# Performance work log

Hardware: AMD Instinct MI355X
Metric: run time of the kernel (lower is better)

## Reference

```python
import jax, jax.numpy as jnp
import numpy as np

N = 20000
E = 500000
IN, HID, OUT = 128, 128, 64
NEG_SLOPE = 0.01  # torch F.leaky_relu default


def setup_inputs() -> dict:
    key = jax.random.key(0)
    ks = jax.random.split(key, 16)
    d = {}
    d['x'] = jax.random.normal(ks[0], (N, IN), dtype=jnp.float32)
    # layer1 per-etype params (torch Linear convention: W is (out,in))
    d['W1_0'] = jax.random.normal(ks[1], (HID, IN), dtype=jnp.float32) / np.sqrt(IN)
    d['b1_0'] = jnp.zeros((HID,), jnp.float32)
    d['a1_0'] = jax.random.normal(ks[2], (2 * HID,), dtype=jnp.float32) / np.sqrt(2 * HID)
    d['W1_1'] = jax.random.normal(ks[3], (HID, IN), dtype=jnp.float32) / np.sqrt(IN)
    d['b1_1'] = jnp.zeros((HID,), jnp.float32)
    d['a1_1'] = jax.random.normal(ks[4], (2 * HID,), dtype=jnp.float32) / np.sqrt(2 * HID)
    # layer2 per-etype params
    d['W2_0'] = jax.random.normal(ks[5], (OUT, HID), dtype=jnp.float32) / np.sqrt(HID)
    d['b2_0'] = jnp.zeros((OUT,), jnp.float32)
    d['a2_0'] = jax.random.normal(ks[6], (2 * OUT,), dtype=jnp.float32) / np.sqrt(2 * OUT)
    d['W2_1'] = jax.random.normal(ks[7], (OUT, HID), dtype=jnp.float32) / np.sqrt(HID)
    d['b2_1'] = jnp.zeros((OUT,), jnp.float32)
    d['a2_1'] = jax.random.normal(ks[8], (2 * OUT,), dtype=jnp.float32) / np.sqrt(2 * OUT)
    # edge lists per etype
    d['src0'] = jax.random.randint(ks[9], (E,), 0, N, dtype=jnp.int32)
    d['dst0'] = jax.random.randint(ks[10], (E,), 0, N, dtype=jnp.int32)
    d['src1'] = jax.random.randint(ks[11], (E,), 0, N, dtype=jnp.int32)
    d['dst1'] = jax.random.randint(ks[12], (E,), 0, N, dtype=jnp.int32)
    return d


def _att_layer(x, Ws, bs, avs, srcs, dsts, n_nodes):
    """One AttHeteroRGCNLayer: per-etype linear + GAT attention + segment
    softmax over destination + weighted sum, then cross-etype sum."""
    h = jnp.zeros((n_nodes, Ws[0].shape[0]), x.dtype)
    for W, b, a, src, dst in zip(Ws, bs, avs, srcs, dsts):
        Wh = x @ W.T + b                       # [N, out]
        out = Wh.shape[1]
        # attn_fc(concat[Wh_src, Wh_dst]) = Wh_src@a_l + Wh_dst@a_r
        al = Wh @ a[:out]                      # [N]
        ar = Wh @ a[out:]                      # [N]
        e = jax.nn.leaky_relu(al[src] + ar[dst], NEG_SLOPE)  # [E]
        # segment softmax over incoming edges of each destination node
        m = jax.ops.segment_max(e, dst, num_segments=n_nodes)  # [N]
        ex = jnp.exp(e - m[dst])
        denom = jax.ops.segment_sum(ex, dst, num_segments=n_nodes)  # [N]
        alpha = ex / denom[dst]                # [E]
        # attention-weighted sum of gathered src messages
        h = h + jax.ops.segment_sum(alpha[:, None] * Wh[src], dst,
                                    num_segments=n_nodes)
    return h


def reference(x, W1_0, b1_0, a1_0, W1_1, b1_1, a1_1,
              W2_0, b2_0, a2_0, W2_1, b2_1, a2_1,
              src0, dst0, src1, dst1):
    srcs = [src0, src1]
    dsts = [dst0, dst1]
    h1 = _att_layer(x, [W1_0, W1_1], [b1_0, b1_1], [a1_0, a1_1], srcs, dsts, N)
    h1 = jax.nn.leaky_relu(h1, NEG_SLOPE)
    h2 = _att_layer(h1, [W2_0, W2_1], [b2_0, b2_1], [a2_0, a2_1], srcs, dsts, N)
    return h2
```

## Files before the change

### kernel.cpp

```cpp
#include <hip/hip_runtime.h>
#include <hip/hip_bf16.h>

#define NNODES 20000
#define NEDGES 500000
#define LRELU(v) ((v) > 0.f ? (v) : (v) * 0.01f)

using bf16_t = __hip_bfloat16;
typedef __attribute__((ext_vector_type(8))) short bf16x8;
typedef __attribute__((ext_vector_type(4))) float f32x4;

__device__ inline float bf2f(short u) {
  unsigned int i = ((unsigned int)(unsigned short)u) << 16;
  float f;
  __builtin_memcpy(&f, &i, 4);
  return f;
}

__global__ __launch_bounds__(256) void k_histpos(const int* __restrict__ dst0,
                                                 const int* __restrict__ dst1,
                                                 int* __restrict__ deg,
                                                 unsigned short* __restrict__ pos0,
                                                 unsigned short* __restrict__ pos1,
                                                 int ne, int n) {
  const int* dst = blockIdx.y ? dst1 : dst0;
  unsigned short* pos = blockIdx.y ? pos1 : pos0;
  int* d = deg + blockIdx.y * n;
  int i = blockIdx.x * 256 + threadIdx.x;
  if (i < ne) pos[i] = (unsigned short)atomicAdd(&d[dst[i]], 1);
}

__global__ __launch_bounds__(1024) void k_scan(const int* __restrict__ deg,
                                               int* __restrict__ row_off,
                                               int n) {
  deg += blockIdx.x * n;
  row_off += blockIdx.x * (n + 1);
  constexpr int PT = 20;
  __shared__ int wsum[16];
  int tid = threadIdx.x, wid = tid >> 6, lane = tid & 63;
  int base_i = tid * PT;
  int v[PT];
  int s = 0;
#pragma unroll
  for (int q = 0; q < PT; ++q) {
    int i = base_i + q;
    v[q] = (i < n) ? deg[i] : 0;
    s += v[q];
  }
  int x = s;
#pragma unroll
  for (int o = 1; o < 64; o <<= 1) {
    int t = __shfl_up(x, o);
    if (lane >= o) x += t;
  }
  if (lane == 63) wsum[wid] = x;
  __syncthreads();
  if (wid == 0) {
    int ws = (lane < 16) ? wsum[lane] : 0;
#pragma unroll
    for (int o = 1; o < 16; o <<= 1) {
      int t = __shfl_up(ws, o);
      if (lane >= o) ws += t;
    }
    if (lane < 16) wsum[lane] = ws;
  }
  __syncthreads();
  int run = (wid ? wsum[wid - 1] : 0) + (x - s);
#pragma unroll
  for (int q = 0; q < PT; ++q) {
    int i = base_i + q;
    if (i < n) row_off[i] = run;
    run += v[q];
  }
  if (tid == 1023) row_off[n] = run;
}

__global__ __launch_bounds__(256) void k_scatter(
    const int* __restrict__ src0, const int* __restrict__ dst0,
    const int* __restrict__ src1, const int* __restrict__ dst1,
    const unsigned short* __restrict__ pos0,
    const unsigned short* __restrict__ pos1, const int* __restrict__ row_off,
    unsigned short* __restrict__ srt0, unsigned short* __restrict__ srt1,
    int ne, int n) {
  const int* src = blockIdx.y ? src1 : src0;
  const int* dst = blockIdx.y ? dst1 : dst0;
  const unsigned short* pos = blockIdx.y ? pos1 : pos0;
  const int* ro = row_off + blockIdx.y * (n + 1);
  unsigned short* srt = blockIdx.y ? srt1 : srt0;
  int i = blockIdx.x * 256 + threadIdx.x;
  if (i < ne) {
    int dd = dst[i];
    srt[ro[dd] + (int)pos[i]] = (unsigned short)src[i];
  }
}

__global__ __launch_bounds__(256) void k_split(const float* __restrict__ in,
                                               bf16_t* __restrict__ hi,
                                               bf16_t* __restrict__ lo,
                                               int n4) {
  int i = blockIdx.x * 256 + threadIdx.x;
  if (i >= n4) return;
  float4 v = *(const float4*)&in[i * 4];
  bf16_t h0 = __float2bfloat16(v.x), h1 = __float2bfloat16(v.y);
  bf16_t h2 = __float2bfloat16(v.z), h3 = __float2bfloat16(v.w);
  hi[i * 4 + 0] = h0;
  hi[i * 4 + 1] = h1;
  hi[i * 4 + 2] = h2;
  hi[i * 4 + 3] = h3;
  lo[i * 4 + 0] = __float2bfloat16(v.x - __bfloat162float(h0));
  lo[i * 4 + 1] = __float2bfloat16(v.y - __bfloat162float(h1));
  lo[i * 4 + 2] = __float2bfloat16(v.z - __bfloat162float(h2));
  lo[i * 4 + 3] = __float2bfloat16(v.w - __bfloat162float(h3));
}

template <int F>
__global__ __launch_bounds__(256) void k_gemm_mfma(
    const bf16_t* __restrict__ Xh, const bf16_t* __restrict__ Xl,
    const bf16_t* __restrict__ Wh0, const bf16_t* __restrict__ Wl0,
    const bf16_t* __restrict__ Wh1, const bf16_t* __restrict__ Wl1,
    const float* __restrict__ b0p, const float* __restrict__ b1p,
    const float* __restrict__ a0p, const float* __restrict__ a1p,
    bf16_t* __restrict__ Y0, bf16_t* __restrict__ Y1, float* __restrict__ al0,
    float* __restrict__ ar0, float* __restrict__ al1, float* __restrict__ ar1,
    int nrows) {
  constexpr int NT = F / 16;
  int t = blockIdx.y;
  const bf16_t* Wgh = t ? Wh1 : Wh0;
  const bf16_t* Wgl = t ? Wl1 : Wl0;
  const float* bias = t ? b1p : b0p;
  const float* av = t ? a1p : a0p;
  bf16_t* Y = t ? Y1 : Y0;
  float* al = t ? al1 : al0;
  float* ar = t ? ar1 : ar0;

  int wid = threadIdx.x >> 6, lane = threadIdx.x & 63;
  int row0 = blockIdx.x * 64 + wid * 16;
  int cl = lane & 15, g4 = lane >> 4;
  int rA = row0 + cl;
  int rAc = min(rA, nrows - 1);

  f32x4 acc[NT] = {};

#pragma unroll
  for (int ks = 0; ks < 4; ++ks) {
    int k0 = ks * 32 + g4 * 8;
    bf16x8 Ah = *(const bf16x8*)&Xh[(size_t)rAc * 128 + k0];
    bf16x8 Al = *(const bf16x8*)&Xl[(size_t)rAc * 128 + k0];
#pragma unroll
    for (int nt = 0; nt < NT; ++nt) {
      size_t off = (size_t)(nt * 16 + cl) * 128 + k0;
      bf16x8 Bh = *(const bf16x8*)&Wgh[off];
      bf16x8 Bl = *(const bf16x8*)&Wgl[off];
      acc[nt] = __builtin_amdgcn_mfma_f32_16x16x32_bf16(Ah, Bh, acc[nt], 0, 0, 0);
      acc[nt] = __builtin_amdgcn_mfma_f32_16x16x32_bf16(Ah, Bl, acc[nt], 0, 0, 0);
      acc[nt] = __builtin_amdgcn_mfma_f32_16x16x32_bf16(Al, Bh, acc[nt], 0, 0, 0);
    }
  }

  float pl[4] = {}, pr[4] = {};
#pragma unroll
  for (int nt = 0; nt < NT; ++nt) {
    int c = nt * 16 + cl;
    float bv = bias[c], aL = av[c], aR = av[F + c];
#pragma unroll
    for (int j = 0; j < 4; ++j) {
      int r = row0 + g4 * 4 + j;
      float v = acc[nt][j] + bv;
      if (r < nrows) Y[(size_t)r * F + c] = __float2bfloat16(v);
      pl[j] += v * aL;
      pr[j] += v * aR;
    }
  }
#pragma unroll
  for (int j = 0; j < 4; ++j) {
    float sl = pl[j], sr = pr[j];
#pragma unroll
    for (int o = 8; o; o >>= 1) {
      sl += __shfl_xor(sl, o);
      sr += __shfl_xor(sr, o);
    }
    int r = row0 + g4 * 4 + j;
    if (cl == 0 && r < nrows) {
      al[r] = sl;
      ar[r] = sr;
    }
  }
}

template <int F, int OMODE>
__global__ __launch_bounds__(256) void k_agg2(
    const int* __restrict__ row_off, const unsigned short* __restrict__ srt0,
    const unsigned short* __restrict__ srt1, const float* __restrict__ al0,
    const float* __restrict__ ar0, const float* __restrict__ al1,
    const float* __restrict__ ar1, const bf16_t* __restrict__ Wg0,
    const bf16_t* __restrict__ Wg1, float* __restrict__ H,
    bf16_t* __restrict__ Hh, bf16_t* __restrict__ Hl, int n) {
  constexpr int LPR = (F * 2) / 16;
  constexpr int NGR = 64 / LPR;
  constexpr int VE = F / LPR;
  int wid = threadIdx.x >> 6, lane = threadIdx.x & 63;
  int d = blockIdx.x * 4 + wid;
  if (d >= n) return;
  int g = lane / LPR, cl = lane % LPR;
  float acc[VE] = {};

#pragma unroll
  for (int t = 0; t < 2; ++t) {
    const int* ro = row_off + t * (n + 1);
    const unsigned short* srt = t ? srt1 : srt0;
    const float* al = t ? al1 : al0;
    const float* ar = t ? ar1 : ar0;
    const bf16_t* Wg = t ? Wg1 : Wg0;
    int beg = ro[d], end = ro[d + 1];
    if (beg == end) continue;
    float ard = ar[d];

    float denT = 0.f;
    float accT[VE] = {};
    int j = beg + g;
    for (; j + NGR < end; j += 2 * NGR) {
      int s0 = srt[j], s1 = srt[j + NGR];
      float e0 = fminf(LRELU(al[s0] + ard), 70.f);
      float e1 = fminf(LRELU(al[s1] + ard), 70.f);
      float w0 = __expf(e0), w1 = __expf(e1);
      denT += w0 + w1;
      bf16x8 r0 = *(const bf16x8*)&Wg[(size_t)s0 * F + cl * 8];
      bf16x8 r1 = *(const bf16x8*)&Wg[(size_t)s1 * F + cl * 8];
#pragma unroll
      for (int v = 0; v < VE; ++v)
        accT[v] += w0 * bf2f(r0[v]) + w1 * bf2f(r1[v]);
    }
    if (j < end) {
      int s0 = srt[j];
      float e0 = fminf(LRELU(al[s0] + ard), 70.f);
      float w0 = __expf(e0);
      denT += w0;
      bf16x8 r0 = *(const bf16x8*)&Wg[(size_t)s0 * F + cl * 8];
#pragma unroll
      for (int v = 0; v < VE; ++v) accT[v] += w0 * bf2f(r0[v]);
    }

#pragma unroll
    for (int o = 32; o >= LPR; o >>= 1) {
      denT += __shfl_xor(denT, o);
#pragma unroll
      for (int v = 0; v < VE; ++v) accT[v] += __shfl_xor(accT[v], o);
    }
    float rden = 1.f / denT;
#pragma unroll
    for (int v = 0; v < VE; ++v) acc[v] += accT[v] * rden;
  }

  if (g == 0) {
    if (OMODE == 0) {
#pragma unroll
      for (int q = 0; q < VE; q += 4) {
        float4 o4 = make_float4(acc[q], acc[q + 1], acc[q + 2], acc[q + 3]);
        *(float4*)&H[(size_t)d * F + cl * VE + q] = o4;
      }
    } else {
      bf16x8 hv, lv;
#pragma unroll
      for (int q = 0; q < VE; ++q) {
        float v = LRELU(acc[q]);
        bf16_t h = __float2bfloat16(v);
        bf16_t l = __float2bfloat16(v - __bfloat162float(h));
        short hb, lb;
        __builtin_memcpy(&hb, &h, 2);
        __builtin_memcpy(&lb, &l, 2);
        hv[q] = hb;
        lv[q] = lb;
      }
      *(bf16x8*)&Hh[(size_t)d * F + cl * 8] = hv;
      *(bf16x8*)&Hl[(size_t)d * F + cl * 8] = lv;
    }
  }
}

extern "C" void kernel_launch(void* const* d_in, const int* in_sizes, int n_in,
                              void* d_out, int out_size, void* d_ws,
                              size_t ws_size, hipStream_t stream) {
  const float* x    = (const float*)d_in[0];
  const float* W1_0 = (const float*)d_in[1];
  const float* b1_0 = (const float*)d_in[2];
  const float* a1_0 = (const float*)d_in[3];
  const float* W1_1 = (const float*)d_in[4];
  const float* b1_1 = (const float*)d_in[5];
  const float* a1_1 = (const float*)d_in[6];
  const float* W2_0 = (const float*)d_in[7];
  const float* b2_0 = (const float*)d_in[8];
  const float* a2_0 = (const float*)d_in[9];
  const float* W2_1 = (const float*)d_in[10];
  const float* b2_1 = (const float*)d_in[11];
  const float* a2_1 = (const float*)d_in[12];
  const int* src0 = (const int*)d_in[13];
  const int* dst0 = (const int*)d_in[14];
  const int* src1 = (const int*)d_in[15];
  const int* dst1 = (const int*)d_in[16];
  float* out = (float*)d_out;

  const int N = NNODES, E = NEDGES;
  typedef unsigned short u16;

  char* w = (char*)d_ws;
  auto alloc = [&](size_t bytes) -> char* {
    char* p = w;
    w += (bytes + 255) & ~(size_t)255;
    return p;
  };
  int* row_off = (int*)alloc(2 * (N + 1) * sizeof(int));
  int* deg     = (int*)alloc(2 * N * sizeof(int));
  u16* pos0    = (u16*)alloc((size_t)E * 2);
  u16* pos1    = (u16*)alloc((size_t)E * 2);
  u16* srt0    = (u16*)alloc((size_t)E * 2);
  u16* srt1    = (u16*)alloc((size_t)E * 2);
  bf16_t* xh   = (bf16_t*)alloc((size_t)N * 128 * 2);
  bf16_t* xl   = (bf16_t*)alloc((size_t)N * 128 * 2);
  bf16_t* Whb_0 = (bf16_t*)alloc((size_t)N * 128 * 2);
  bf16_t* Whb_1 = (bf16_t*)alloc((size_t)N * 128 * 2);
  bf16_t* h1h  = (bf16_t*)alloc((size_t)N * 128 * 2);
  bf16_t* h1l  = (bf16_t*)alloc((size_t)N * 128 * 2);
  bf16_t* w1h0 = (bf16_t*)alloc(128 * 128 * 2);
  bf16_t* w1l0 = (bf16_t*)alloc(128 * 128 * 2);
  bf16_t* w1h1 = (bf16_t*)alloc(128 * 128 * 2);
  bf16_t* w1l1 = (bf16_t*)alloc(128 * 128 * 2);
  bf16_t* w2h0 = (bf16_t*)alloc(64 * 128 * 2);
  bf16_t* w2l0 = (bf16_t*)alloc(64 * 128 * 2);
  bf16_t* w2h1 = (bf16_t*)alloc(64 * 128 * 2);
  bf16_t* w2l1 = (bf16_t*)alloc(64 * 128 * 2);
  bf16_t* Wh2b_0 = (bf16_t*)alloc((size_t)N * 64 * 2);
  bf16_t* Wh2b_1 = (bf16_t*)alloc((size_t)N * 64 * 2);
  float* alA   = (float*)alloc(N * sizeof(float));
  float* arA   = (float*)alloc(N * sizeof(float));
  float* alB   = (float*)alloc(N * sizeof(float));
  float* arB   = (float*)alloc(N * sizeof(float));
  (void)ws_size;

  hipMemsetAsync(deg, 0, 2 * N * sizeof(int), stream);
  dim3 eg((E + 255) / 256, 2);
  k_histpos<<<eg, 256, 0, stream>>>(dst0, dst1, deg, pos0, pos1, E, N);
  k_scan<<<2, 1024, 0, stream>>>(deg, row_off, N);
  k_scatter<<<eg, 256, 0, stream>>>(src0, dst0, src1, dst1, pos0, pos1,
                                    row_off, srt0, srt1, E, N);

  k_split<<<(N * 128 / 4 + 255) / 256, 256, 0, stream>>>(x, xh, xl, N * 128 / 4);
  k_split<<<(128 * 128 / 4 + 255) / 256, 256, 0, stream>>>(W1_0, w1h0, w1l0, 128 * 128 / 4);
  k_split<<<(128 * 128 / 4 + 255) / 256, 256, 0, stream>>>(W1_1, w1h1, w1l1, 128 * 128 / 4);
  k_split<<<(64 * 128 / 4 + 255) / 256, 256, 0, stream>>>(W2_0, w2h0, w2l0, 64 * 128 / 4);
  k_split<<<(64 * 128 / 4 + 255) / 256, 256, 0, stream>>>(W2_1, w2h1, w2l1, 64 * 128 / 4);

  int ngrid4 = (N + 3) / 4;
  dim3 gg((N + 63) / 64, 2);

  k_gemm_mfma<128><<<gg, 256, 0, stream>>>(
      xh, xl, w1h0, w1l0, w1h1, w1l1, b1_0, b1_1, a1_0, a1_1, Whb_0, Whb_1,
      alA, arA, alB, arB, N);
  k_agg2<128, 1><<<ngrid4, 256, 0, stream>>>(
      row_off, srt0, srt1, alA, arA, alB, arB, Whb_0, Whb_1, nullptr, h1h,
      h1l, N);

  k_gemm_mfma<64><<<gg, 256, 0, stream>>>(
      h1h, h1l, w2h0, w2l0, w2h1, w2l1, b2_0, b2_1, a2_0, a2_1, Wh2b_0,
      Wh2b_1, alA, arA, alB, arB, N);
  k_agg2<64, 0><<<ngrid4, 256, 0, stream>>>(
      row_off, srt0, srt1, alA, arA, alB, arB, Wh2b_0, Wh2b_1, out, nullptr,
      nullptr, N);
}
```

Baseline: 274.4 us.

## Merge independent preprocessing and layer-1 GEMM kernels into fewer launches

```diff
diff --git a/kernel.cpp b/kernel.cpp
--- a/kernel.cpp
+++ b/kernel.cpp
@@ -6,6 +6,7 @@
 #define LRELU(v) ((v) > 0.f ? (v) : (v) * 0.01f)
 
 using bf16_t = __hip_bfloat16;
+typedef unsigned short u16;
 typedef __attribute__((ext_vector_type(8))) short bf16x8;
 typedef __attribute__((ext_vector_type(4))) float f32x4;
 
@@ -16,88 +17,24 @@
   return f;
 }
 
-__global__ __launch_bounds__(256) void k_histpos(const int* __restrict__ dst0,
-                                                 const int* __restrict__ dst1,
-                                                 int* __restrict__ deg,
-                                                 unsigned short* __restrict__ pos0,
-                                                 unsigned short* __restrict__ pos1,
-                                                 int ne, int n) {
-  const int* dst = blockIdx.y ? dst1 : dst0;
-  unsigned short* pos = blockIdx.y ? pos1 : pos0;
-  int* d = deg + blockIdx.y * n;
-  int i = blockIdx.x * 256 + threadIdx.x;
-  if (i < ne) pos[i] = (unsigned short)atomicAdd(&d[dst[i]], 1);
-}
-
-__global__ __launch_bounds__(1024) void k_scan(const int* __restrict__ deg,
-                                               int* __restrict__ row_off,
-                                               int n) {
-  deg += blockIdx.x * n;
-  row_off += blockIdx.x * (n + 1);
-  constexpr int PT = 20;
-  __shared__ int wsum[16];
-  int tid = threadIdx.x, wid = tid >> 6, lane = tid & 63;
-  int base_i = tid * PT;
-  int v[PT];
-  int s = 0;
-#pragma unroll
-  for (int q = 0; q < PT; ++q) {
-    int i = base_i + q;
-    v[q] = (i < n) ? deg[i] : 0;
-    s += v[q];
-  }
-  int x = s;
-#pragma unroll
-  for (int o = 1; o < 64; o <<= 1) {
-    int t = __shfl_up(x, o);
-    if (lane >= o) x += t;
-  }
-  if (lane == 63) wsum[wid] = x;
-  __syncthreads();
-  if (wid == 0) {
-    int ws = (lane < 16) ? wsum[lane] : 0;
-#pragma unroll
-    for (int o = 1; o < 16; o <<= 1) {
-      int t = __shfl_up(ws, o);
-      if (lane >= o) ws += t;
-    }
-    if (lane < 16) wsum[lane] = ws;
-  }
-  __syncthreads();
-  int run = (wid ? wsum[wid - 1] : 0) + (x - s);
-#pragma unroll
-  for (int q = 0; q < PT; ++q) {
-    int i = base_i + q;
-    if (i < n) row_off[i] = run;
-    run += v[q];
-  }
-  if (tid == 1023) row_off[n] = run;
-}
-
-__global__ __launch_bounds__(256) void k_scatter(
-    const int* __restrict__ src0, const int* __restrict__ dst0,
-    const int* __restrict__ src1, const int* __restrict__ dst1,
-    const unsigned short* __restrict__ pos0,
-    const unsigned short* __restrict__ pos1, const int* __restrict__ row_off,
-    unsigned short* __restrict__ srt0, unsigned short* __restrict__ srt1,
-    int ne, int n) {
-  const int* src = blockIdx.y ? src1 : src0;
-  const int* dst = blockIdx.y ? dst1 : dst0;
-  const unsigned short* pos = blockIdx.y ? pos1 : pos0;
-  const int* ro = row_off + blockIdx.y * (n + 1);
-  unsigned short* srt = blockIdx.y ? srt1 : srt0;
-  int i = blockIdx.x * 256 + threadIdx.x;
-  if (i < ne) {
-    int dd = dst[i];
-    srt[ro[dd] + (int)pos[i]] = (unsigned short)src[i];
-  }
-}
-
-__global__ __launch_bounds__(256) void k_split(const float* __restrict__ in,
-                                               bf16_t* __restrict__ hi,
-                                               bf16_t* __restrict__ lo,
-                                               int n4) {
-  int i = blockIdx.x * 256 + threadIdx.x;
+constexpr int HB = (NEDGES + 255) / 256;
+constexpr int SBX = (NNODES * 128 / 4 + 255) / 256;
+constexpr int SBW1 = (128 * 128 / 4 + 255) / 256;
+constexpr int SBW2 = (64 * 128 / 4 + 255) / 256;
+constexpr int GB = (NNODES + 63) / 64;
+
+__device__ inline void histpos_body(int bb, int t, const int* dst0,
+                                    const int* dst1, int* deg, u16* pos0,
+                                    u16* pos1) {
+  const int* dst = t ? dst1 : dst0;
+  u16* pos = t ? pos1 : pos0;
+  int* d = deg + t * NNODES;
+  int i = bb * 256 + threadIdx.x;
+  if (i < NEDGES) pos[i] = (u16)atomicAdd(&d[dst[i]], 1);
+}
+
+__device__ inline void split_body(const float* in, bf16_t* hi, bf16_t* lo,
+                                  int i, int n4) {
   if (i >= n4) return;
   float4 v = *(const float4*)&in[i * 4];
   bf16_t h0 = __float2bfloat16(v.x), h1 = __float2bfloat16(v.y);
@@ -112,18 +49,30 @@
   lo[i * 4 + 3] = __float2bfloat16(v.w - __bfloat162float(h3));
 }
 
+__device__ inline void scatter_body(int bb, int t, const int* src0,
+                                    const int* dst0, const int* src1,
+                                    const int* dst1, const u16* pos0,
+                                    const u16* pos1, const int* row_off,
+                                    u16* srt0, u16* srt1) {
+  const int* src = t ? src1 : src0;
+  const int* dst = t ? dst1 : dst0;
+  const u16* pos = t ? pos1 : pos0;
+  const int* ro = row_off + t * (NNODES + 1);
+  u16* srt = t ? srt1 : srt0;
+  int i = bb * 256 + threadIdx.x;
+  if (i < NEDGES) {
+    int dd = dst[i];
+    srt[ro[dd] + (int)pos[i]] = (u16)src[i];
+  }
+}
+
 template <int F>
-__global__ __launch_bounds__(256) void k_gemm_mfma(
-    const bf16_t* __restrict__ Xh, const bf16_t* __restrict__ Xl,
-    const bf16_t* __restrict__ Wh0, const bf16_t* __restrict__ Wl0,
-    const bf16_t* __restrict__ Wh1, const bf16_t* __restrict__ Wl1,
-    const float* __restrict__ b0p, const float* __restrict__ b1p,
-    const float* __restrict__ a0p, const float* __restrict__ a1p,
-    bf16_t* __restrict__ Y0, bf16_t* __restrict__ Y1, float* __restrict__ al0,
-    float* __restrict__ ar0, float* __restrict__ al1, float* __restrict__ ar1,
-    int nrows) {
+__device__ inline void gemm_body(
+    int bx, int t, const bf16_t* Xh, const bf16_t* Xl, const bf16_t* Wh0,
+    const bf16_t* Wl0, const bf16_t* Wh1, const bf16_t* Wl1, const float* b0p,
+    const float* b1p, const float* a0p, const float* a1p, bf16_t* Y0,
+    bf16_t* Y1, float* al0, float* ar0, float* al1, float* ar1, int nrows) {
   constexpr int NT = F / 16;
-  int t = blockIdx.y;
   const bf16_t* Wgh = t ? Wh1 : Wh0;
   const bf16_t* Wgl = t ? Wl1 : Wl0;
   const float* bias = t ? b1p : b0p;
@@ -133,10 +82,9 @@
   float* ar = t ? ar1 : ar0;
 
   int wid = threadIdx.x >> 6, lane = threadIdx.x & 63;
-  int row0 = blockIdx.x * 64 + wid * 16;
+  int row0 = bx * 64 + wid * 16;
   int cl = lane & 15, g4 = lane >> 4;
-  int rA = row0 + cl;
-  int rAc = min(rA, nrows - 1);
+  int rAc = min(row0 + cl, nrows - 1);
 
   f32x4 acc[NT] = {};
 
@@ -186,10 +134,122 @@
   }
 }
 
+__global__ __launch_bounds__(256) void k_pre(
+    const int* __restrict__ dst0, const int* __restrict__ dst1,
+    int* __restrict__ deg, u16* __restrict__ pos0, u16* __restrict__ pos1,
+    const float* __restrict__ x, bf16_t* __restrict__ xh,
+    bf16_t* __restrict__ xl, const float* __restrict__ W1_0,
+    bf16_t* __restrict__ w1h0, bf16_t* __restrict__ w1l0,
+    const float* __restrict__ W1_1, bf16_t* __restrict__ w1h1,
+    bf16_t* __restrict__ w1l1, const float* __restrict__ W2_0,
+    bf16_t* __restrict__ w2h0, bf16_t* __restrict__ w2l0,
+    const float* __restrict__ W2_1, bf16_t* __restrict__ w2h1,
+    bf16_t* __restrict__ w2l1) {
+  int b = blockIdx.x;
+  if (b < 2 * HB) {
+    histpos_body(b >= HB ? b - HB : b, b >= HB, dst0, dst1, deg, pos0, pos1);
+    return;
+  }
+  b -= 2 * HB;
+  int tid = threadIdx.x;
+  if (b < SBX) { split_body(x, xh, xl, b * 256 + tid, NNODES * 128 / 4); return; }
+  b -= SBX;
+  if (b < SBW1) { split_body(W1_0, w1h0, w1l0, b * 256 + tid, 128 * 128 / 4); return; }
+  b -= SBW1;
+  if (b < SBW1) { split_body(W1_1, w1h1, w1l1, b * 256 + tid, 128 * 128 / 4); return; }
+  b -= SBW1;
+  if (b < SBW2) { split_body(W2_0, w2h0, w2l0, b * 256 + tid, 64 * 128 / 4); return; }
+  b -= SBW2;
+  split_body(W2_1, w2h1, w2l1, b * 256 + tid, 64 * 128 / 4);
+}
+
+__global__ __launch_bounds__(1024) void k_scan(const int* __restrict__ deg,
+                                               int* __restrict__ row_off,
+                                               int n) {
+  deg += blockIdx.x * n;
+  row_off += blockIdx.x * (n + 1);
+  constexpr int PT = 20;
+  __shared__ int wsum[16];
+  int tid = threadIdx.x, wid = tid >> 6, lane = tid & 63;
+  int base_i = tid * PT;
+  int v[PT];
+  int s = 0;
+#pragma unroll
+  for (int q = 0; q < PT; ++q) {
+    int i = base_i + q;
+    v[q] = (i < n) ? deg[i] : 0;
+    s += v[q];
+  }
+  int x = s;
+#pragma unroll
+  for (int o = 1; o < 64; o <<= 1) {
+    int t = __shfl_up(x, o);
+    if (lane >= o) x += t;
+  }
+  if (lane == 63) wsum[wid] = x;
+  __syncthreads();
+  if (wid == 0) {
+    int ws = (lane < 16) ? wsum[lane] : 0;
+#pragma unroll
+    for (int o = 1; o < 16; o <<= 1) {
+      int t = __shfl_up(ws, o);
+      if (lane >= o) ws += t;
+    }
+    if (lane < 16) wsum[lane] = ws;
+  }
+  __syncthreads();
+  int run = (wid ? wsum[wid - 1] : 0) + (x - s);
+#pragma unroll
+  for (int q = 0; q < PT; ++q) {
+    int i = base_i + q;
+    if (i < n) row_off[i] = run;
+    run += v[q];
+  }
+  if (tid == 1023) row_off[n] = run;
+}
+
+__global__ __launch_bounds__(256) void k_mid(
+    const bf16_t* __restrict__ xh, const bf16_t* __restrict__ xl,
+    const bf16_t* __restrict__ w1h0, const bf16_t* __restrict__ w1l0,
+    const bf16_t* __restrict__ w1h1, const bf16_t* __restrict__ w1l1,
+    const float* __restrict__ b1_0, const float* __restrict__ b1_1,
+    const float* __restrict__ a1_0, const float* __restrict__ a1_1,
+    bf16_t* __restrict__ Whb_0, bf16_t* __restrict__ Whb_1,
+    float* __restrict__ alA, float* __restrict__ arA, float* __restrict__ alB,
+    float* __restrict__ arB, const int* __restrict__ src0,
+    const int* __restrict__ dst0, const int* __restrict__ src1,
+    const int* __restrict__ dst1, const u16* __restrict__ pos0,
+    const u16* __restrict__ pos1, const int* __restrict__ row_off,
+    u16* __restrict__ srt0, u16* __restrict__ srt1) {
+  int b = blockIdx.x;
+  if (b < 2 * GB) {
+    gemm_body<128>(b >= GB ? b - GB : b, b >= GB, xh, xl, w1h0, w1l0, w1h1,
+                   w1l1, b1_0, b1_1, a1_0, a1_1, Whb_0, Whb_1, alA, arA, alB,
+                   arB, NNODES);
+    return;
+  }
+  b -= 2 * GB;
+  scatter_body(b >= HB ? b - HB : b, b >= HB, src0, dst0, src1, dst1, pos0,
+               pos1, row_off, srt0, srt1);
+}
+
+__global__ __launch_bounds__(256) void k_gemm64(
+    const bf16_t* __restrict__ Xh, const bf16_t* __restrict__ Xl,
+    const bf16_t* __restrict__ w2h0, const bf16_t* __restrict__ w2l0,
+    const bf16_t* __restrict__ w2h1, const bf16_t* __restrict__ w2l1,
+    const float* __restrict__ b2_0, const float* __restrict__ b2_1,
+    const float* __restrict__ a2_0, const float* __restrict__ a2_1,
+    bf16_t* __restrict__ Y0, bf16_t* __restrict__ Y1, float* __restrict__ al0,
+    float* __restrict__ ar0, float* __restrict__ al1,
+    float* __restrict__ ar1) {
+  gemm_body<64>(blockIdx.x, blockIdx.y, Xh, Xl, w2h0, w2l0, w2h1, w2l1, b2_0,
+                b2_1, a2_0, a2_1, Y0, Y1, al0, ar0, al1, ar1, NNODES);
+}
+
 template <int F, int OMODE>
 __global__ __launch_bounds__(256) void k_agg2(
-    const int* __restrict__ row_off, const unsigned short* __restrict__ srt0,
-    const unsigned short* __restrict__ srt1, const float* __restrict__ al0,
+    const int* __restrict__ row_off, const u16* __restrict__ srt0,
+    const u16* __restrict__ srt1, const float* __restrict__ al0,
     const float* __restrict__ ar0, const float* __restrict__ al1,
     const float* __restrict__ ar1, const bf16_t* __restrict__ Wg0,
     const bf16_t* __restrict__ Wg1, float* __restrict__ H,
@@ -206,7 +266,7 @@
 #pragma unroll
   for (int t = 0; t < 2; ++t) {
     const int* ro = row_off + t * (n + 1);
-    const unsigned short* srt = t ? srt1 : srt0;
+    const u16* srt = t ? srt1 : srt0;
     const float* al = t ? al1 : al0;
     const float* ar = t ? ar1 : ar0;
     const bf16_t* Wg = t ? Wg1 : Wg0;
@@ -299,7 +359,6 @@
   float* out = (float*)d_out;
 
   const int N = NNODES, E = NEDGES;
-  typedef unsigned short u16;
 
   char* w = (char*)d_ws;
   auto alloc = [&](size_t bytes) -> char* {
@@ -336,31 +395,24 @@
   (void)ws_size;
 
   hipMemsetAsync(deg, 0, 2 * N * sizeof(int), stream);
-  dim3 eg((E + 255) / 256, 2);
-  k_histpos<<<eg, 256, 0, stream>>>(dst0, dst1, deg, pos0, pos1, E, N);
+
+  int preg = 2 * HB + SBX + 2 * SBW1 + 2 * SBW2;
+  k_pre<<<preg, 256, 0, stream>>>(dst0, dst1, deg, pos0, pos1, x, xh, xl,
+                                  W1_0, w1h0, w1l0, W1_1, w1h1, w1l1, W2_0,
+                                  w2h0, w2l0, W2_1, w2h1, w2l1);
   k_scan<<<2, 1024, 0, stream>>>(deg, row_off, N);
-  k_scatter<<<eg, 256, 0, stream>>>(src0, dst0, src1, dst1, pos0, pos1,
-                                    row_off, srt0, srt1, E, N);
-
-  k_split<<<(N * 128 / 4 + 255) / 256, 256, 0, stream>>>(x, xh, xl, N * 128 / 4);
-  k_split<<<(128 * 128 / 4 + 255) / 256, 256, 0, stream>>>(W1_0, w1h0, w1l0, 128 * 128 / 4);
-  k_split<<<(128 * 128 / 4 + 255) / 256, 256, 0, stream>>>(W1_1, w1h1, w1l1, 128 * 128 / 4);
-  k_split<<<(64 * 128 / 4 + 255) / 256, 256, 0, stream>>>(W2_0, w2h0, w2l0, 64 * 128 / 4);
-  k_split<<<(64 * 128 / 4 + 255) / 256, 256, 0, stream>>>(W2_1, w2h1, w2l1, 64 * 128 / 4);
-
+  int midg = 2 * GB + 2 * HB;
+  k_mid<<<midg, 256, 0, stream>>>(xh, xl, w1h0, w1l0, w1h1, w1l1, b1_0, b1_1,
+                                  a1_0, a1_1, Whb_0, Whb_1, alA, arA, alB,
+                                  arB, src0, dst0, src1, dst1, pos0, pos1,
+                                  row_off, srt0, srt1);
   int ngrid4 = (N + 3) / 4;
-  dim3 gg((N + 63) / 64, 2);
-
-  k_gemm_mfma<128><<<gg, 256, 0, stream>>>(
-      xh, xl, w1h0, w1l0, w1h1, w1l1, b1_0, b1_1, a1_0, a1_1, Whb_0, Whb_1,
-      alA, arA, alB, arB, N);
   k_agg2<128, 1><<<ngrid4, 256, 0, stream>>>(
       row_off, srt0, srt1, alA, arA, alB, arB, Whb_0, Whb_1, nullptr, h1h,
       h1l, N);
-
-  k_gemm_mfma<64><<<gg, 256, 0, stream>>>(
-      h1h, h1l, w2h0, w2l0, w2h1, w2l1, b2_0, b2_1, a2_0, a2_1, Wh2b_0,
-      Wh2b_1, alA, arA, alB, arB, N);
+  k_gemm64<<<dim3(GB, 2), 256, 0, stream>>>(h1h, h1l, w2h0, w2l0, w2h1, w2l1,
+                                            b2_0, b2_1, a2_0, a2_1, Wh2b_0,
+                                            Wh2b_1, alA, arA, alB, arB);
   k_agg2<64, 0><<<ngrid4, 256, 0, stream>>>(
       row_off, srt0, srt1, alA, arA, alB, arB, Wh2b_0, Wh2b_1, out, nullptr,
       nullptr, N);
```

Result: faster. 257.3 us (-6.2%).
